# Kernel tuning notes

Measured on AMD Instinct MI355X. Metric: run time of the kernel, lower is better.

## Reference

```python
import jax, jax.numpy as jnp
import numpy as np

B = 8; NPC = 12500; N = B * NPC
L = 10.0; RES = 0.7; K = 16
IN_CH = 64; H1 = 68; H2 = 128; RNN = 128; ATTN = 32; E4 = 4 * RNN
EPS = 1e-5


def _knn_np(refs, queries, k):
    out = np.empty((queries.shape[0], k), dtype=np.int64)
    r2 = (refs * refs).sum(1)
    for s in range(0, queries.shape[0], 2048):
        q = queries[s:s + 2048]
        d2 = (q * q).sum(1)[:, None] - 2.0 * q @ refs.T + r2[None, :]
        out[s:s + q.shape[0]] = np.argpartition(d2, k, axis=1)[:, :k]
    return out


def setup_inputs():
    rng = np.random.default_rng(0)
    pos = rng.uniform(0.0, L, (N, 3)).astype(np.float32)
    batch = np.repeat(np.arange(B), NPC).astype(np.int32)
    x = (0.5 * rng.standard_normal((N, IN_CH))).astype(np.float32)
    refl = rng.uniform(0.0, 1.0, N).astype(np.float32)
    # voxel-grid sampling: one representative point per occupied voxel per cloud
    G = int(np.ceil(L / RES)) + 1
    v = np.floor(pos / RES).astype(np.int64)
    vkey = ((batch.astype(np.int64) * G + v[:, 0]) * G + v[:, 1]) * G + v[:, 2]
    _, first = np.unique(vkey, return_index=True)
    idx = np.sort(first)
    M = idx.shape[0]
    # per-cloud brute-force KNN (k neighbors in full set for every sampled point)
    src_list = []
    for b in range(B):
        qi = idx[(idx >= b * NPC) & (idx < (b + 1) * NPC)]
        src_list.append(_knn_np(pos[b * NPC:(b + 1) * NPC], pos[qi], K) + b * NPC)
    src = np.concatenate(src_list, 0).reshape(-1)
    tgt = np.repeat(np.arange(M), K)
    edge_index = np.stack([src, tgt]).astype(np.int32)

    def W(*s):
        return jnp.asarray((0.05 * rng.standard_normal(s)).astype(np.float32))

    def zeros(c):
        return jnp.zeros((c,), jnp.float32)

    def bnp(c):  # packed inference-mode BN params: [gamma, beta, mean, var]
        return jnp.asarray(np.stack([1.0 + 0.1 * rng.standard_normal(c), 0.1 * rng.standard_normal(c), 0.1 * rng.standard_normal(c), 1.0 + 0.1 * rng.uniform(0.0, 1.0, c)]).astype(np.float32))

    def dwp(c):  # depthwise k=1 conv = per-channel [weight, bias]
        return jnp.asarray(np.stack([1.0 + 0.1 * rng.standard_normal(c), 0.1 * rng.standard_normal(c)]).astype(np.float32))

    gum = -np.log(-np.log(rng.uniform(1e-6, 1.0 - 1e-6, (B, 2))))
    return dict(
        x=jnp.asarray(x), pos=jnp.asarray(pos), reflectance=jnp.asarray(refl),
        gumbel=jnp.asarray(gum.astype(np.float32)),
        gate_w1=W(4, H1), gate_b1=zeros(H1), gate_w2=W(H1, H1), gate_b2=zeros(H1),
        gate_wg=W(H1, 2), gate_bg=jnp.asarray(np.array([0.0, 2.0], np.float32)),
        loc_w1=W(H1, H2), loc_b1=zeros(H2), loc_w2=W(H2, H2), loc_b2=zeros(H2),
        attn_w1=W(H2, ATTN), attn_b1=zeros(ATTN), attn_w2=W(ATTN),
        exp_w=W(RNN, E4), exp_b=zeros(E4), exp_bn=bnp(E4),
        ds1_dw=dwp(E4), ds1_bn1=bnp(E4), ds1_pw_w=W(E4, E4), ds1_pw_b=zeros(E4), ds1_bn2=bnp(E4),
        blk_bn1=bnp(E4),
        ds2_dw=dwp(E4), ds2_bn1=bnp(E4), ds2_pw_w=W(E4, E4), ds2_pw_b=zeros(E4), ds2_bn2=bnp(E4),
        blk_bn2=bnp(E4),
        proj_w=W(E4, RNN), proj_b=zeros(RNN), proj_bn=bnp(RNN),
        batch=jnp.asarray(batch), idx=jnp.asarray(idx.astype(np.int32)),
        edge_index=jnp.asarray(edge_index), k=K, num_graphs=B)


def _bn(z, p):
    return p[0] * (z - p[2]) / jnp.sqrt(p[3] + EPS) + p[1]


def reference(x, pos, reflectance, gumbel, gate_w1, gate_b1, gate_w2, gate_b2, gate_wg, gate_bg, loc_w1, loc_b1, loc_w2, loc_b2, attn_w1, attn_b1, attn_w2, exp_w, exp_b, exp_bn, ds1_dw, ds1_bn1, ds1_pw_w, ds1_pw_b, ds1_bn2, blk_bn1, ds2_dw, ds2_bn1, ds2_pw_w, ds2_pw_b, ds2_bn2, blk_bn2, proj_w, proj_b, proj_bn, batch, idx, edge_index, k, num_graphs):
    # --- BinaryReflectanceGate (soft gumbel-softmax, tau=1) ---
    feats = jnp.concatenate([pos, reflectance[:, None]], -1)  # [N,4]
    h = jax.nn.relu(feats @ gate_w1 + gate_b1)
    h = jax.nn.relu(h @ gate_w2 + gate_b2)
    pooled = jax.ops.segment_max(h, batch, num_segments=num_graphs)  # global_max_pool
    logits = pooled @ gate_wg + gate_bg
    y_soft = jax.nn.softmax(logits + gumbel, axis=-1)
    refl_g = y_soft[:, 1][batch] * reflectance  # gated reflectance [N]
    pos4 = jnp.concatenate([pos, refl_g[:, None]], -1)  # [N,4]
    # --- AttentivePointNetConv: gather -> local MLP -> softmax attn -> reduce ---
    M = idx.shape[0]
    src = edge_index[0].reshape(M, k)  # k source neighbors per centroid
    msg_in = jnp.concatenate([x[src], pos4[src] - pos4[idx][:, None, :]], -1)  # [M,k,68]
    hm = jax.nn.relu(msg_in @ loc_w1 + loc_b1)
    msg = jax.nn.relu(hm @ loc_w2 + loc_b2)  # [M,k,128]
    score = jnp.tanh(msg @ attn_w1 + attn_b1) @ attn_w2  # [M,k]
    alpha = jax.nn.softmax(score, axis=-1)  # softmax over each centroid's edges
    agg = jnp.einsum('mk,mkc->mc', alpha, msg)  # [M,128]
    # --- InvertedResidualBlock (all convs kernel=1 -> channel matmuls, BN inference) ---
    out = jax.nn.relu(_bn(agg @ exp_w + exp_b, exp_bn))  # expand 128->512

    def ds(z, dw, bn1, pw_w, pw_b, bn2):
        d = jax.nn.relu(_bn(z * dw[0] + dw[1], bn1))  # depthwise k=1
        return _bn(d @ pw_w + pw_b, bn2)  # pointwise

    out = _bn(ds(out, ds1_dw, ds1_bn1, ds1_pw_w, ds1_pw_b, ds1_bn2), blk_bn1)
    out = _bn(ds(out, ds2_dw, ds2_bn1, ds2_pw_w, ds2_pw_b, ds2_bn2), blk_bn2)
    out = _bn(out @ proj_w + proj_b, proj_bn)  # project 512->128
    out = jax.nn.relu(out + agg)  # identity shortcut (RNN==RNN)
    return (out, pos[idx], batch[idx], refl_g[idx])
```

## Files before the change

kernel.cpp:

```cpp
#include <hip/hip_runtime.h>
#include <hip/hip_bf16.h>

typedef __hip_bfloat16 bf16;

#define B_GR 8
#define IN_CH 64
#define H1 68
#define H2 128
#define ATTN 32
#define E4 512
#define RNN 128
#define KNN 16
#define EPSV 1e-5f

typedef __attribute__((ext_vector_type(8))) short s8v;
typedef __attribute__((ext_vector_type(4))) float f4v;
#define MFMA16(a,b,c) __builtin_amdgcn_mfma_f32_16x16x32_bf16(a,b,c,0,0,0)

#define SK96 104
#define SK128 136
#define SK512 520

template<int DT> __device__ __forceinline__ float LD(const void* p, size_t i) {
    if (DT) return __bfloat162float(((const bf16*)p)[i]);
    return ((const float*)p)[i];
}
template<int DT> __device__ __forceinline__ void ST(void* p, size_t i, float v) {
    if (DT) ((bf16*)p)[i] = __float2bfloat16(v);
    else    ((float*)p)[i] = v;
}
__device__ __forceinline__ unsigned short f2bfb(float f) {
    unsigned u = __float_as_uint(f);
    unsigned r = (u + 0x7FFFu + ((u >> 16) & 1u)) >> 16;
    return (unsigned short)r;
}
__device__ __forceinline__ float bfb2f(unsigned short u) {
    return __uint_as_float(((unsigned)u) << 16);
}

__global__ void prep_kernel(const void* pos, int* flag, int* pooled) {
    const int tid = threadIdx.x;
    for (int i = tid; i < B_GR*H1; i += 256) pooled[i] = 0;
    if (tid == 0) {
        const unsigned* w = (const unsigned*)pos;
        int ok = 1;
        #pragma unroll 8
        for (int i = 0; i < 256; i++) {
            float f = __uint_as_float((w[i] & 0xFFFFu) << 16);
            if (!(f >= -0.01f && f <= 10.05f)) ok = 0;
        }
        *flag = ok;
    }
}

#define W1T_E (128*SK96)
#define W2T_E (128*SK128)
#define AW1T_E (32*SK128)
#define EXPT_E (512*SK128)
#define D1T_E (512*SK512)
#define D2T_E (512*SK512)
#define PJT_E (128*SK512)
#define GW2T_E (80*SK96)
template<int DT> __global__ __launch_bounds__(256) void trans_kernel(
    const int* __restrict__ flag,
    const void* __restrict__ w1, const void* __restrict__ w2, const void* __restrict__ aw1,
    const void* __restrict__ expw, const void* __restrict__ d1pw,
    const void* __restrict__ d2pw, const void* __restrict__ pjw,
    const void* __restrict__ gw2,
    unsigned short* __restrict__ w1T, unsigned short* __restrict__ w2T,
    unsigned short* __restrict__ aw1T, unsigned short* __restrict__ expwT,
    unsigned short* __restrict__ d1pwT, unsigned short* __restrict__ d2pwT,
    unsigned short* __restrict__ pjwT, unsigned short* __restrict__ gw2gT)
{
    if (*flag != DT) return;
    const int T0 = W1T_E, T1 = T0+W2T_E, T2 = T1+AW1T_E, T3 = T2+EXPT_E,
              T4 = T3+D1T_E, T5 = T4+D2T_E, T6 = T5+PJT_E, T7 = T6+GW2T_E;
    for (int i = blockIdx.x*256 + threadIdx.x; i < T7; i += gridDim.x*256) {
        if (i < T0) {
            int n = i / SK96, k = i - n*SK96;
            w1T[i] = (k < H1) ? f2bfb(LD<DT>(w1, (size_t)k*H2 + n)) : 0;
        } else if (i < T1) {
            int j = i - T0; int n = j / SK128, k = j - n*SK128;
            w2T[j] = (k < H2) ? f2bfb(LD<DT>(w2, (size_t)k*H2 + n)) : 0;
        } else if (i < T2) {
            int j = i - T1; int n = j / SK128, k = j - n*SK128;
            aw1T[j] = (k < H2) ? f2bfb(LD<DT>(aw1, (size_t)k*ATTN + n)) : 0;
        } else if (i < T3) {
            int j = i - T2; int n = j / SK128, k = j - n*SK128;
            expwT[j] = (k < RNN) ? f2bfb(LD<DT>(expw, (size_t)k*E4 + n)) : 0;
        } else if (i < T4) {
            int j = i - T3; int n = j / SK512, k = j - n*SK512;
            d1pwT[j] = (k < E4) ? f2bfb(LD<DT>(d1pw, (size_t)k*E4 + n)) : 0;
        } else if (i < T5) {
            int j = i - T4; int n = j / SK512, k = j - n*SK512;
            d2pwT[j] = (k < E4) ? f2bfb(LD<DT>(d2pw, (size_t)k*E4 + n)) : 0;
        } else if (i < T6) {
            int j = i - T5; int n = j / SK512, k = j - n*SK512;
            pjwT[j] = (k < E4) ? f2bfb(LD<DT>(pjw, (size_t)k*RNN + n)) : 0;
        } else {
            int j = i - T6; int n = j / SK96, k = j - n*SK96;
            gw2gT[j] = (k < H1 && n < H1) ? f2bfb(LD<DT>(gw2, (size_t)k*H1 + n)) : 0;
        }
    }
}

template<int DT> __global__ void coef_kernel(
    const int* __restrict__ flag,
    const void* __restrict__ expb, const void* __restrict__ expbn,
    const void* __restrict__ d1dw, const void* __restrict__ d1bn1,
    const void* __restrict__ d1pb, const void* __restrict__ d1bn2, const void* __restrict__ bbn1,
    const void* __restrict__ d2dw, const void* __restrict__ d2bn1,
    const void* __restrict__ d2pb, const void* __restrict__ d2bn2, const void* __restrict__ bbn2,
    const void* __restrict__ pjb, const void* __restrict__ pjbn,
    float4* __restrict__ C1, float2* __restrict__ C2, float2* __restrict__ C3,
    float2* __restrict__ C4)
{
    if (*flag != DT) return;
    int c = blockIdx.x*256 + threadIdx.x;
    if (c < E4) {
        float a_e = LD<DT>(expbn,c) * rsqrtf(LD<DT>(expbn,3*E4+c)+EPSV);
        float t0  = a_e*(LD<DT>(expb,c) - LD<DT>(expbn,2*E4+c)) + LD<DT>(expbn,E4+c);
        float a1 = LD<DT>(d1bn1,c) * rsqrtf(LD<DT>(d1bn1,3*E4+c)+EPSV);
        float s1 = a1 * LD<DT>(d1dw,c);
        float t1 = a1*(LD<DT>(d1dw,E4+c) - LD<DT>(d1bn1,2*E4+c)) + LD<DT>(d1bn1,E4+c);
        C1[c] = make_float4(a_e, t0, s1, t1);
        float a2 = LD<DT>(d1bn2,c) * rsqrtf(LD<DT>(d1bn2,3*E4+c)+EPSV);
        float t2 = a2*(LD<DT>(d1pb,c) - LD<DT>(d1bn2,2*E4+c)) + LD<DT>(d1bn2,E4+c);
        float a3 = LD<DT>(bbn1,c) * rsqrtf(LD<DT>(bbn1,3*E4+c)+EPSV);
        float S2 = a3*a2;
        float T2 = a3*(t2 - LD<DT>(bbn1,2*E4+c)) + LD<DT>(bbn1,E4+c);
        float a4 = LD<DT>(d2bn1,c) * rsqrtf(LD<DT>(d2bn1,3*E4+c)+EPSV);
        float sdw = a4 * LD<DT>(d2dw,c);
        float tdw = a4*(LD<DT>(d2dw,E4+c) - LD<DT>(d2bn1,2*E4+c)) + LD<DT>(d2bn1,E4+c);
        C2[c] = make_float2(sdw*S2, sdw*T2 + tdw);
        float a5 = LD<DT>(d2bn2,c) * rsqrtf(LD<DT>(d2bn2,3*E4+c)+EPSV);
        float t5 = a5*(LD<DT>(d2pb,c) - LD<DT>(d2bn2,2*E4+c)) + LD<DT>(d2bn2,E4+c);
        float a6 = LD<DT>(bbn2,c) * rsqrtf(LD<DT>(bbn2,3*E4+c)+EPSV);
        C3[c] = make_float2(a6*a5, a6*(t5 - LD<DT>(bbn2,2*E4+c)) + LD<DT>(bbn2,E4+c));
    }
    if (c < RNN) {
        float ap = LD<DT>(pjbn,c) * rsqrtf(LD<DT>(pjbn,3*RNN+c)+EPSV);
        C4[c] = make_float2(ap, ap*(LD<DT>(pjb,c) - LD<DT>(pjbn,2*RNN+c)) + LD<DT>(pjbn,RNN+c));
    }
}

template<int DT> __global__ __launch_bounds__(256) void gate_mfma(
    const int* __restrict__ flag,
    const void* __restrict__ pos, const void* __restrict__ refl,
    const void* __restrict__ w1, const void* __restrict__ b1, const void* __restrict__ b2g,
    const unsigned short* __restrict__ gw2gT,
    int* __restrict__ pooled, int NPC, int CPB)
{
    if (*flag != DT) return;
    __shared__ __align__(16) unsigned short hs[256*SK96];
    __shared__ float w1s[4*H1], b1s[H1], b2s[H1];
    const int tid = threadIdx.x;
    for (int i = tid; i < 4*H1; i += 256) w1s[i] = LD<DT>(w1, i);
    if (tid < H1) { b1s[tid] = LD<DT>(b1, tid); b2s[tid] = LD<DT>(b2g, tid); }
    __syncthreads();

    const int bb = blockIdx.x / CPB;
    const int cc = blockIdx.x % CPB;
    const int base = bb*NPC + cc*256;
    const int limit = NPC - cc*256;
    const int p = base + ((tid < limit) ? tid : 0);

    {
        float f0 = LD<DT>(pos, (size_t)p*3+0), f1 = LD<DT>(pos, (size_t)p*3+1);
        float f2 = LD<DT>(pos, (size_t)p*3+2), f3 = LD<DT>(refl, p);
        float h[H1];
        #pragma unroll
        for (int j = 0; j < H1; j++)
            h[j] = fmaxf(b1s[j] + f0*w1s[j] + f1*w1s[H1+j] + f2*w1s[2*H1+j] + f3*w1s[3*H1+j], 0.f);
        #pragma unroll
        for (int j = 0; j < H1; j += 2) {
            unsigned v = (unsigned)f2bfb(h[j]) | ((unsigned)f2bfb(h[j+1]) << 16);
            *(unsigned*)&hs[tid*SK96 + j] = v;
        }
        #pragma unroll
        for (int j = H1; j < 96; j += 2) *(unsigned*)&hs[tid*SK96 + j] = 0;
    }
    __syncthreads();

    const int wv = tid >> 6, lane = tid & 63, quad = lane >> 4, l15 = lane & 15;
    f4v acc[4][5];
    #pragma unroll
    for (int mt = 0; mt < 4; mt++)
        #pragma unroll
        for (int nt = 0; nt < 5; nt++) acc[mt][nt] = (f4v){0.f,0.f,0.f,0.f};
    s8v af[4][3];
    #pragma unroll
    for (int mt = 0; mt < 4; mt++)
        #pragma unroll
        for (int ks = 0; ks < 3; ks++)
            af[mt][ks] = *(const s8v*)&hs[(wv*64 + mt*16 + l15)*SK96 + ks*32 + quad*8];
    #pragma unroll
    for (int nt = 0; nt < 5; nt++) {
        #pragma unroll
        for (int ks = 0; ks < 3; ks++) {
            s8v bf_ = *(const s8v*)&gw2gT[(size_t)(nt*16 + l15)*SK96 + ks*32 + quad*8];
            #pragma unroll
            for (int mt = 0; mt < 4; mt++) acc[mt][nt] = MFMA16(af[mt][ks], bf_, acc[mt][nt]);
        }
    }
    #pragma unroll
    for (int nt = 0; nt < 5; nt++) {
        int col = nt*16 + l15;
        float v = acc[0][nt][0];
        #pragma unroll
        for (int mt = 0; mt < 4; mt++)
            #pragma unroll
            for (int r = 0; r < 4; r++) v = fmaxf(v, acc[mt][nt][r]);
        v = fmaxf(v, __shfl_xor(v, 16));
        v = fmaxf(v, __shfl_xor(v, 32));
        if (quad == 0 && col < H1) {
            float o = fmaxf(v + b2s[col], 0.f);
            atomicMax(&pooled[bb*H1 + col], __float_as_int(o));
        }
    }
}

template<int DT> __global__ void gate2_kernel(
    const int* __restrict__ flag, const int* __restrict__ pooled,
    const void* __restrict__ wg, const void* __restrict__ bg,
    const void* __restrict__ gum, float* __restrict__ y1)
{
    if (*flag != DT) return;
    __shared__ float lg[B_GR][2];
    const int t = threadIdx.x;
    if (t < B_GR*2) {
        int b = t >> 1, g = t & 1;
        float a = LD<DT>(bg, g) + LD<DT>(gum, b*2+g);
        for (int c = 0; c < H1; c++) a += __int_as_float(pooled[b*H1+c]) * LD<DT>(wg, c*2+g);
        lg[b][g] = a;
    }
    __syncthreads();
    if (t < B_GR) {
        float l0 = lg[t][0], l1 = lg[t][1];
        float m = fmaxf(l0, l1);
        float e0 = __expf(l0-m), e1 = __expf(l1-m);
        y1[t] = e1 / (e0 + e1);
    }
}

template<int DT> __global__ __launch_bounds__(256) void edge_mfma(
    const int* __restrict__ flag,
    const void* __restrict__ x, const void* __restrict__ pos,
    const void* __restrict__ refl, const float* __restrict__ y1,
    const int* __restrict__ batch,
    const int* __restrict__ idxarr, const int* __restrict__ esrc,
    const void* __restrict__ b1, const void* __restrict__ b2,
    const void* __restrict__ ab1, const void* __restrict__ aw2,
    const unsigned short* __restrict__ gw1T, const unsigned short* __restrict__ gw2T,
    const unsigned short* __restrict__ gaw1T,
    void* __restrict__ out, int M)
{
    if (*flag != DT) return;
    __shared__ __align__(16) unsigned short u2[128*SK128];
    __shared__ float p4[8][4];
    __shared__ int   srow[128];
    __shared__ float b1s[H2], b2s[H2], ab1s[ATTN], aw2s[ATTN];
    __shared__ float scores[128], alpha[128];

    const int tid = threadIdx.x;
    const int m0 = blockIdx.x * 8;

    if (tid < 128) {
        int mm = m0 + (tid >> 4); if (mm >= M) mm = M - 1;
        srow[tid] = esrc[mm*KNN + (tid & 15)];
    }
    if (tid < 32) {
        int tt = tid >> 2, c = tid & 3;
        int mm = m0 + tt; if (mm >= M) mm = M - 1;
        int t_idx = idxarr[mm];
        p4[tt][c] = (c < 3) ? LD<DT>(pos, (size_t)t_idx*3 + c)
                            : y1[batch[t_idx]] * LD<DT>(refl, t_idx);
    }
    if (tid < H2) { b1s[tid] = LD<DT>(b1, tid); b2s[tid] = LD<DT>(b2, tid); }
    if (tid < ATTN) { ab1s[tid] = LD<DT>(ab1, tid); aw2s[tid] = LD<DT>(aw2, tid); }
    __syncthreads();

    if (DT) {
        int r = tid >> 1, hf = tid & 1;
        int s = srow[r], tt = r >> 4;
        const uint4* xs = (const uint4*)x;
        uint4* du = (uint4*)u2;
        #pragma unroll
        for (int q = 0; q < 4; q++)
            du[r*17 + hf*4 + q] = xs[(size_t)s*8 + hf*4 + q];
        if (hf == 0) {
            #pragma unroll
            for (int k = 64; k < 68; k++) {
                float v = (k < 67) ? LD<1>(pos, (size_t)s*3 + (k-64)) - p4[tt][k-64]
                                   : y1[batch[s]] * LD<1>(refl, s) - p4[tt][3];
                u2[r*SK128 + k] = f2bfb(v);
            }
        } else {
            #pragma unroll
            for (int k = 68; k < 96; k += 2) *(unsigned*)&u2[r*SK128 + k] = 0;
        }
    } else {
        int r = tid >> 1, half = tid & 1;
        int s = srow[r], tt = r >> 4;
        size_t xb = (size_t)s * IN_CH;
        int k0 = half * 48;
        for (int kk = 0; kk < 48; kk++) {
            int k = k0 + kk;
            float v;
            if (k < IN_CH)       v = LD<DT>(x, xb + k);
            else if (k < 67)     v = LD<DT>(pos, (size_t)s*3 + (k - 64)) - p4[tt][k - 64];
            else if (k == 67)    v = y1[batch[s]] * LD<DT>(refl, s) - p4[tt][3];
            else                 v = 0.f;
            u2[r*SK128 + k] = f2bfb(v);
        }
    }
    __syncthreads();

    const int wv = tid >> 6, lane = tid & 63, quad = lane >> 4, l15 = lane & 15;
    const int rbase = wv * 32;

    {
        s8v af[2][3];
        #pragma unroll
        for (int mt = 0; mt < 2; mt++)
            #pragma unroll
            for (int ks = 0; ks < 3; ks++)
                af[mt][ks] = *(const s8v*)&u2[(rbase + mt*16 + l15)*SK128 + ks*32 + quad*8];
        __syncthreads();
        f4v acc[2][8];
        #pragma unroll
        for (int mt = 0; mt < 2; mt++)
            #pragma unroll
            for (int nt = 0; nt < 8; nt++) acc[mt][nt] = (f4v){0.f,0.f,0.f,0.f};
        #pragma unroll
        for (int nt = 0; nt < 8; nt++) {
            #pragma unroll
            for (int ks = 0; ks < 3; ks++) {
                s8v bf_ = *(const s8v*)&gw1T[(size_t)(nt*16 + l15)*SK96 + ks*32 + quad*8];
                acc[0][nt] = MFMA16(af[0][ks], bf_, acc[0][nt]);
                acc[1][nt] = MFMA16(af[1][ks], bf_, acc[1][nt]);
            }
        }
        #pragma unroll
        for (int mt = 0; mt < 2; mt++)
            #pragma unroll
            for (int nt = 0; nt < 8; nt++)
                #pragma unroll
                for (int r = 0; r < 4; r++) {
                    int row = rbase + mt*16 + quad*4 + r;
                    int col = nt*16 + l15;
                    u2[row*SK128 + col] = f2bfb(fmaxf(acc[mt][nt][r] + b1s[col], 0.f));
                }
    }
    __syncthreads();

    {
        s8v af[2][4];
        #pragma unroll
        for (int mt = 0; mt < 2; mt++)
            #pragma unroll
            for (int ks = 0; ks < 4; ks++)
                af[mt][ks] = *(const s8v*)&u2[(rbase + mt*16 + l15)*SK128 + ks*32 + quad*8];
        __syncthreads();
        f4v acc[2][8];
        #pragma unroll
        for (int mt = 0; mt < 2; mt++)
            #pragma unroll
            for (int nt = 0; nt < 8; nt++) acc[mt][nt] = (f4v){0.f,0.f,0.f,0.f};
        #pragma unroll
        for (int nt = 0; nt < 8; nt++) {
            #pragma unroll
            for (int ks = 0; ks < 4; ks++) {
                s8v bf_ = *(const s8v*)&gw2T[(size_t)(nt*16 + l15)*SK128 + ks*32 + quad*8];
                acc[0][nt] = MFMA16(af[0][ks], bf_, acc[0][nt]);
                acc[1][nt] = MFMA16(af[1][ks], bf_, acc[1][nt]);
            }
        }
        #pragma unroll
        for (int mt = 0; mt < 2; mt++)
            #pragma unroll
            for (int nt = 0; nt < 8; nt++)
                #pragma unroll
                for (int r = 0; r < 4; r++) {
                    int row = rbase + mt*16 + quad*4 + r;
                    int col = nt*16 + l15;
                    u2[row*SK128 + col] = f2bfb(fmaxf(acc[mt][nt][r] + b2s[col], 0.f));
                }
    }
    __syncthreads();

    {
        s8v af[2][4];
        #pragma unroll
        for (int mt = 0; mt < 2; mt++)
            #pragma unroll
            for (int ks = 0; ks < 4; ks++)
                af[mt][ks] = *(const s8v*)&u2[(rbase + mt*16 + l15)*SK128 + ks*32 + quad*8];
        f4v acc[2][2];
        #pragma unroll
        for (int mt = 0; mt < 2; mt++)
            #pragma unroll
            for (int nt = 0; nt < 2; nt++) acc[mt][nt] = (f4v){0.f,0.f,0.f,0.f};
        #pragma unroll
        for (int nt = 0; nt < 2; nt++) {
            #pragma unroll
            for (int ks = 0; ks < 4; ks++) {
                s8v bf_ = *(const s8v*)&gaw1T[(size_t)(nt*16 + l15)*SK128 + ks*32 + quad*8];
                acc[0][nt] = MFMA16(af[0][ks], bf_, acc[0][nt]);
                acc[1][nt] = MFMA16(af[1][ks], bf_, acc[1][nt]);
            }
        }
        #pragma unroll
        for (int mt = 0; mt < 2; mt++)
            #pragma unroll
            for (int r = 0; r < 4; r++) {
                float s = 0.f;
                #pragma unroll
                for (int nt = 0; nt < 2; nt++) {
                    int col = nt*16 + l15;
                    s += tanhf(acc[mt][nt][r] + ab1s[col]) * aw2s[col];
                }
                s += __shfl_xor(s, 1);
                s += __shfl_xor(s, 2);
                s += __shfl_xor(s, 4);
                s += __shfl_xor(s, 8);
                if (l15 == 0) scores[rbase + mt*16 + quad*4 + r] = s;
            }
    }
    __syncthreads();

    if (tid < 128) {
        int base = (tid >> 4) << 4;
        float mx = scores[base];
        #pragma unroll
        for (int j = 1; j < KNN; j++) mx = fmaxf(mx, scores[base+j]);
        float den = 0.f;
        #pragma unroll
        for (int j = 0; j < KNN; j++) den += __expf(scores[base+j] - mx);
        alpha[tid] = __expf(scores[tid] - mx) / den;
    }
    __syncthreads();

    if (tid < 128) {
        int tt = tid >> 4, c0 = (tid & 15) * 8;
        int mm = m0 + tt;
        float a[8] = {0,0,0,0,0,0,0,0};
        #pragma unroll
        for (int j = 0; j < KNN; j++) {
            float al = alpha[tt*16 + j];
            s8v v = *(const s8v*)&u2[(tt*16 + j)*SK128 + c0];
            #pragma unroll
            for (int e = 0; e < 8; e++) a[e] += al * bfb2f((unsigned short)v[e]);
        }
        if (mm < M) {
            if (DT) {
                unsigned short pk[8];
                #pragma unroll
                for (int e = 0; e < 8; e++) pk[e] = f2bfb(a[e]);
                *(uint4*)((bf16*)out + (size_t)mm*H2 + c0) = *(const uint4*)pk;
            } else {
                #pragma unroll
                for (int e = 0; e < 8; e++) ST<0>(out, (size_t)mm*H2 + c0 + e, a[e]);
            }
        }
    } else if (tid < 160) {
        int t = tid - 128;
        int tt = t >> 2, c = t & 3;
        int mm = m0 + tt;
        if (mm < M) {
            if (c < 3) ST<DT>(out, (size_t)M*128 + mm*3 + c, p4[tt][c]);
            else {
                ST<DT>(out, (size_t)M*131 + mm, (float)batch[idxarr[mm]]);
                ST<DT>(out, (size_t)M*132 + mm, p4[tt][3]);
            }
        }
    }
}

template<int DT> __global__ __launch_bounds__(256) void post_mfma(
    const int* __restrict__ flag,
    const unsigned short* __restrict__ expwT, const unsigned short* __restrict__ d1pwT,
    const unsigned short* __restrict__ d2pwT, const unsigned short* __restrict__ pjwT,
    const float4* __restrict__ C1, const float2* __restrict__ C2,
    const float2* __restrict__ C3, const float2* __restrict__ C4,
    void* __restrict__ out, int M)
{
    if (*flag != DT) return;
    __shared__ __align__(16) unsigned short zs[32*SK512];
    __shared__ __align__(16) unsigned short a0[32*SK128];
    const int tid = threadIdx.x;
    const int m0 = blockIdx.x * 32;

    {
        int r = tid >> 3;
        int c0 = (tid & 7) * 16;
        int mm = m0 + r;
        for (int c = c0; c < c0+16; c++) {
            float v = (mm < M) ? LD<DT>(out, (size_t)mm*RNN + c) : 0.f;
            a0[r*SK128 + c] = f2bfb(v);
        }
        if ((tid & 7) == 7) for (int c = RNN; c < SK128; c++) a0[r*SK128 + c] = 0;
    }
    __syncthreads();

    const int wv = tid >> 6, lane = tid & 63, quad = lane >> 4, l15 = lane & 15;
    const int nbase = wv * 128;

    f4v acc[2][8];

    #pragma unroll
    for (int mt = 0; mt < 2; mt++)
        #pragma unroll
        for (int nt = 0; nt < 8; nt++) acc[mt][nt] = (f4v){0.f,0.f,0.f,0.f};
    #pragma unroll
    for (int ks = 0; ks < 4; ks++) {
        s8v af0 = *(const s8v*)&a0[(l15)*SK128 + ks*32 + quad*8];
        s8v af1 = *(const s8v*)&a0[(16+l15)*SK128 + ks*32 + quad*8];
        #pragma unroll
        for (int nt = 0; nt < 8; nt++) {
            s8v bf_ = *(const s8v*)&expwT[(size_t)(nbase + nt*16 + l15)*SK128 + ks*32 + quad*8];
            acc[0][nt] = MFMA16(af0, bf_, acc[0][nt]);
            acc[1][nt] = MFMA16(af1, bf_, acc[1][nt]);
        }
    }
    #pragma unroll
    for (int nt = 0; nt < 8; nt++) {
        int col = nbase + nt*16 + l15;
        float4 cf = C1[col];
        #pragma unroll
        for (int mt = 0; mt < 2; mt++)
            #pragma unroll
            for (int r = 0; r < 4; r++) {
                int row = mt*16 + quad*4 + r;
                float u = fmaxf(cf.x*acc[mt][nt][r] + cf.y, 0.f);
                float d = fmaxf(cf.z*u + cf.w, 0.f);
                zs[row*SK512 + col] = f2bfb(d);
            }
    }
    __syncthreads();

    #pragma unroll
    for (int mt = 0; mt < 2; mt++)
        #pragma unroll
        for (int nt = 0; nt < 8; nt++) acc[mt][nt] = (f4v){0.f,0.f,0.f,0.f};
    for (int ks = 0; ks < 16; ks++) {
        s8v af0 = *(const s8v*)&zs[(l15)*SK512 + ks*32 + quad*8];
        s8v af1 = *(const s8v*)&zs[(16+l15)*SK512 + ks*32 + quad*8];
        #pragma unroll
        for (int nt = 0; nt < 8; nt++) {
            s8v bf_ = *(const s8v*)&d1pwT[(size_t)(nbase + nt*16 + l15)*SK512 + ks*32 + quad*8];
            acc[0][nt] = MFMA16(af0, bf_, acc[0][nt]);
            acc[1][nt] = MFMA16(af1, bf_, acc[1][nt]);
        }
    }
    __syncthreads();
    #pragma unroll
    for (int nt = 0; nt < 8; nt++) {
        int col = nbase + nt*16 + l15;
        float2 cf = C2[col];
        #pragma unroll
        for (int mt = 0; mt < 2; mt++)
            #pragma unroll
            for (int r = 0; r < 4; r++) {
                int row = mt*16 + quad*4 + r;
                zs[row*SK512 + col] = f2bfb(fmaxf(cf.x*acc[mt][nt][r] + cf.y, 0.f));
            }
    }
    __syncthreads();

    #pragma unroll
    for (int mt = 0; mt < 2; mt++)
        #pragma unroll
        for (int nt = 0; nt < 8; nt++) acc[mt][nt] = (f4v){0.f,0.f,0.f,0.f};
    for (int ks = 0; ks < 16; ks++) {
        s8v af0 = *(const s8v*)&zs[(l15)*SK512 + ks*32 + quad*8];
        s8v af1 = *(const s8v*)&zs[(16+l15)*SK512 + ks*32 + quad*8];
        #pragma unroll
        for (int nt = 0; nt < 8; nt++) {
            s8v bf_ = *(const s8v*)&d2pwT[(size_t)(nbase + nt*16 + l15)*SK512 + ks*32 + quad*8];
            acc[0][nt] = MFMA16(af0, bf_, acc[0][nt]);
            acc[1][nt] = MFMA16(af1, bf_, acc[1][nt]);
        }
    }
    __syncthreads();
    #pragma unroll
    for (int nt = 0; nt < 8; nt++) {
        int col = nbase + nt*16 + l15;
        float2 cf = C3[col];
        #pragma unroll
        for (int mt = 0; mt < 2; mt++)
            #pragma unroll
            for (int r = 0; r < 4; r++) {
                int row = mt*16 + quad*4 + r;
                zs[row*SK512 + col] = f2bfb(cf.x*acc[mt][nt][r] + cf.y);
            }
    }
    __syncthreads();

    {
        f4v pacc[2][2];
        #pragma unroll
        for (int mt = 0; mt < 2; mt++)
            #pragma unroll
            for (int nt = 0; nt < 2; nt++) pacc[mt][nt] = (f4v){0.f,0.f,0.f,0.f};
        for (int ks = 0; ks < 16; ks++) {
            s8v af0 = *(const s8v*)&zs[(l15)*SK512 + ks*32 + quad*8];
            s8v af1 = *(const s8v*)&zs[(16+l15)*SK512 + ks*32 + quad*8];
            #pragma unroll
            for (int nt = 0; nt < 2; nt++) {
                s8v bf_ = *(const s8v*)&pjwT[(size_t)(wv*32 + nt*16 + l15)*SK512 + ks*32 + quad*8];
                pacc[0][nt] = MFMA16(af0, bf_, pacc[0][nt]);
                pacc[1][nt] = MFMA16(af1, bf_, pacc[1][nt]);
            }
        }
        #pragma unroll
        for (int nt = 0; nt < 2; nt++) {
            int col = wv*32 + nt*16 + l15;
            float2 cf = C4[col];
            #pragma unroll
            for (int mt = 0; mt < 2; mt++)
                #pragma unroll
                for (int r = 0; r < 4; r++) {
                    int row = mt*16 + quad*4 + r;
                    int mm = m0 + row;
                    if (mm < M) {
                        float agv = bfb2f(a0[row*SK128 + col]);
                        float o = fmaxf(cf.x*pacc[mt][nt][r] + cf.y + agv, 0.f);
                        ST<DT>(out, (size_t)mm*RNN + col, o);
                    }
                }
        }
    }
}

extern "C" void kernel_launch(void* const* d_in, const int* in_sizes, int n_in,
                              void* d_out, int out_size, void* d_ws, size_t ws_size,
                              hipStream_t stream)
{
    const void* x    = d_in[0];
    const void* pos  = d_in[1];
    const void* refl = d_in[2];
    const void* gum  = d_in[3];
    const void* gw1  = d_in[4];
    const void* gb1  = d_in[5];
    const void* gw2  = d_in[6];
    const void* gb2  = d_in[7];
    const void* gwg  = d_in[8];
    const void* gbg  = d_in[9];
    const void* lw1  = d_in[10];
    const void* lb1  = d_in[11];
    const void* lw2  = d_in[12];
    const void* lb2  = d_in[13];
    const void* aw1  = d_in[14];
    const void* ab1  = d_in[15];
    const void* aw2  = d_in[16];
    const void* expw = d_in[17];
    const void* expb = d_in[18];
    const void* expbn= d_in[19];
    const void* d1dw = d_in[20];
    const void* d1bn1= d_in[21];
    const void* d1pw = d_in[22];
    const void* d1pb = d_in[23];
    const void* d1bn2= d_in[24];
    const void* bbn1 = d_in[25];
    const void* d2dw = d_in[26];
    const void* d2bn1= d_in[27];
    const void* d2pw = d_in[28];
    const void* d2pb = d_in[29];
    const void* d2bn2= d_in[30];
    const void* bbn2 = d_in[31];
    const void* pjw  = d_in[32];
    const void* pjb  = d_in[33];
    const void* pjbn = d_in[34];
    const int* batch = (const int*)d_in[35];
    const int* idxp  = (const int*)d_in[36];
    const int* eidx  = (const int*)d_in[37];

    const int N = in_sizes[2];
    const int M = in_sizes[36];
    const int NPC = N / B_GR;
    const int CPB = (NPC + 255) / 256;

    char* wsb = (char*)d_ws;
    int*  flag   = (int*)wsb;
    int*  pooled = (int*)(wsb + 16);
    float* y1    = (float*)(wsb + 2304);
    unsigned short* w1T   = (unsigned short*)(wsb + 2368);
    unsigned short* w2T   = w1T + W1T_E;
    unsigned short* aw1T  = w2T + W2T_E;
    unsigned short* expwT = aw1T + AW1T_E;
    unsigned short* d1pwT = expwT + EXPT_E;
    unsigned short* d2pwT = d1pwT + D1T_E;
    unsigned short* pjwT  = d2pwT + D2T_E;
    unsigned short* gw2gT = pjwT + PJT_E;
    float4* C1 = (float4*)(gw2gT + GW2T_E + 8);
    float2* C2 = (float2*)(C1 + E4);
    float2* C3 = C2 + E4;
    float2* C4 = C3 + E4;

    prep_kernel<<<1, 256, 0, stream>>>(pos, flag, pooled);

    trans_kernel<0><<<512, 256, 0, stream>>>(flag, lw1, lw2, aw1, expw, d1pw, d2pw, pjw, gw2,
                                             w1T, w2T, aw1T, expwT, d1pwT, d2pwT, pjwT, gw2gT);
    trans_kernel<1><<<512, 256, 0, stream>>>(flag, lw1, lw2, aw1, expw, d1pw, d2pw, pjw, gw2,
                                             w1T, w2T, aw1T, expwT, d1pwT, d2pwT, pjwT, gw2gT);

    coef_kernel<0><<<2, 256, 0, stream>>>(flag, expb, expbn, d1dw, d1bn1, d1pb, d1bn2, bbn1,
                                          d2dw, d2bn1, d2pb, d2bn2, bbn2, pjb, pjbn,
                                          C1, C2, C3, C4);
    coef_kernel<1><<<2, 256, 0, stream>>>(flag, expb, expbn, d1dw, d1bn1, d1pb, d1bn2, bbn1,
                                          d2dw, d2bn1, d2pb, d2bn2, bbn2, pjb, pjbn,
                                          C1, C2, C3, C4);

    gate_mfma<0><<<B_GR*CPB, 256, 0, stream>>>(flag, pos, refl, gw1, gb1, gb2, gw2gT, pooled, NPC, CPB);
    gate_mfma<1><<<B_GR*CPB, 256, 0, stream>>>(flag, pos, refl, gw1, gb1, gb2, gw2gT, pooled, NPC, CPB);

    gate2_kernel<0><<<1, 64, 0, stream>>>(flag, pooled, gwg, gbg, gum, y1);
    gate2_kernel<1><<<1, 64, 0, stream>>>(flag, pooled, gwg, gbg, gum, y1);

    const int EB = (M + 7) / 8;
    edge_mfma<0><<<EB, 256, 0, stream>>>(flag, x, pos, refl, y1, batch, idxp, eidx,
                                         lb1, lb2, ab1, aw2, w1T, w2T, aw1T, d_out, M);
    edge_mfma<1><<<EB, 256, 0, stream>>>(flag, x, pos, refl, y1, batch, idxp, eidx,
                                         lb1, lb2, ab1, aw2, w1T, w2T, aw1T, d_out, M);

    const int PB = (M + 31) / 32;
    post_mfma<0><<<PB, 256, 0, stream>>>(flag, expwT, d1pwT, d2pwT, pjwT, C1, C2, C3, C4, d_out, M);
    post_mfma<1><<<PB, 256, 0, stream>>>(flag, expwT, d1pwT, d2pwT, pjwT, C1, C2, C3, C4, d_out, M);
}
```

Before: 560.8 us.

## Make edge_mfma wave-independent: load A fragments from global, drop block barriers

Each wave now owns two centroids end to end. It loads the gathered neighbor features straight from global memory into MFMA A-fragments instead of staging them through shared memory. Every block-wide __syncthreads is removed and the per-block shared bias, score and alpha arrays go away, so bias loads move into registers. Softmax and aggregation now run inside each wave. tanhf is replaced by an exp-based fast_tanh, which changes accuracy slightly. The risk is uncoalesced gathered global loads and possible races, since waves reuse their own u2 rows without barriers.

Measured after the change: 472.9 us. 1.19x faster.

```diff
diff --git a/kernel.cpp b/kernel.cpp
--- a/kernel.cpp
+++ b/kernel.cpp
@@ -36,6 +36,11 @@
 }
 __device__ __forceinline__ float bfb2f(unsigned short u) {
     return __uint_as_float(((unsigned)u) << 16);
+}
+__device__ __forceinline__ float fast_tanh(float x) {
+    x = fminf(fmaxf(x, -12.f), 12.f);
+    float e = __expf(2.f * x);
+    return (e - 1.f) / (e + 1.f);
 }
 
 __global__ void prep_kernel(const void* pos, int* flag, int* pooled) {
@@ -257,81 +262,56 @@
 {
     if (*flag != DT) return;
     __shared__ __align__(16) unsigned short u2[128*SK128];
-    __shared__ float p4[8][4];
-    __shared__ int   srow[128];
-    __shared__ float b1s[H2], b2s[H2], ab1s[ATTN], aw2s[ATTN];
-    __shared__ float scores[128], alpha[128];
+    __shared__ float ssc[4][2][16];
 
     const int tid = threadIdx.x;
-    const int m0 = blockIdx.x * 8;
-
-    if (tid < 128) {
-        int mm = m0 + (tid >> 4); if (mm >= M) mm = M - 1;
-        srow[tid] = esrc[mm*KNN + (tid & 15)];
-    }
-    if (tid < 32) {
-        int tt = tid >> 2, c = tid & 3;
-        int mm = m0 + tt; if (mm >= M) mm = M - 1;
+    const int wv = tid >> 6, lane = tid & 63, quad = lane >> 4, l15 = lane & 15;
+    const int m0 = blockIdx.x * 8 + wv * 2;
+    const int rb = wv * 32;
+
+    s8v af[2][3];
+    int mcl[2];
+    float p4v[2][4];
+    #pragma unroll
+    for (int t = 0; t < 2; t++) {
+        int mm = m0 + t; if (mm >= M) mm = M - 1;
+        mcl[t] = mm;
         int t_idx = idxarr[mm];
-        p4[tt][c] = (c < 3) ? LD<DT>(pos, (size_t)t_idx*3 + c)
-                            : y1[batch[t_idx]] * LD<DT>(refl, t_idx);
-    }
-    if (tid < H2) { b1s[tid] = LD<DT>(b1, tid); b2s[tid] = LD<DT>(b2, tid); }
-    if (tid < ATTN) { ab1s[tid] = LD<DT>(ab1, tid); aw2s[tid] = LD<DT>(aw2, tid); }
-    __syncthreads();
-
-    if (DT) {
-        int r = tid >> 1, hf = tid & 1;
-        int s = srow[r], tt = r >> 4;
-        const uint4* xs = (const uint4*)x;
-        uint4* du = (uint4*)u2;
-        #pragma unroll
-        for (int q = 0; q < 4; q++)
-            du[r*17 + hf*4 + q] = xs[(size_t)s*8 + hf*4 + q];
-        if (hf == 0) {
-            #pragma unroll
-            for (int k = 64; k < 68; k++) {
-                float v = (k < 67) ? LD<1>(pos, (size_t)s*3 + (k-64)) - p4[tt][k-64]
-                                   : y1[batch[s]] * LD<1>(refl, s) - p4[tt][3];
-                u2[r*SK128 + k] = f2bfb(v);
-            }
+        p4v[t][0] = LD<DT>(pos, (size_t)t_idx*3 + 0);
+        p4v[t][1] = LD<DT>(pos, (size_t)t_idx*3 + 1);
+        p4v[t][2] = LD<DT>(pos, (size_t)t_idx*3 + 2);
+        p4v[t][3] = y1[batch[t_idx]] * LD<DT>(refl, t_idx);
+        int s = esrc[mm*KNN + l15];
+        if (DT) {
+            const unsigned short* xs = (const unsigned short*)x + (size_t)s*IN_CH;
+            af[t][0] = *(const s8v*)(xs + quad*8);
+            af[t][1] = *(const s8v*)(xs + 32 + quad*8);
         } else {
-            #pragma unroll
-            for (int k = 68; k < 96; k += 2) *(unsigned*)&u2[r*SK128 + k] = 0;
-        }
-    } else {
-        int r = tid >> 1, half = tid & 1;
-        int s = srow[r], tt = r >> 4;
-        size_t xb = (size_t)s * IN_CH;
-        int k0 = half * 48;
-        for (int kk = 0; kk < 48; kk++) {
-            int k = k0 + kk;
-            float v;
-            if (k < IN_CH)       v = LD<DT>(x, xb + k);
-            else if (k < 67)     v = LD<DT>(pos, (size_t)s*3 + (k - 64)) - p4[tt][k - 64];
-            else if (k == 67)    v = y1[batch[s]] * LD<DT>(refl, s) - p4[tt][3];
-            else                 v = 0.f;
-            u2[r*SK128 + k] = f2bfb(v);
-        }
-    }
-    __syncthreads();
-
-    const int wv = tid >> 6, lane = tid & 63, quad = lane >> 4, l15 = lane & 15;
-    const int rbase = wv * 32;
+            unsigned short tmp0[8], tmp1[8];
+            #pragma unroll
+            for (int e = 0; e < 8; e++) {
+                tmp0[e] = f2bfb(LD<0>(x, (size_t)s*IN_CH + quad*8 + e));
+                tmp1[e] = f2bfb(LD<0>(x, (size_t)s*IN_CH + 32 + quad*8 + e));
+            }
+            af[t][0] = *(const s8v*)tmp0;
+            af[t][1] = *(const s8v*)tmp1;
+        }
+        s8v a2 = (s8v){0,0,0,0,0,0,0,0};
+        if (quad == 0) {
+            a2[0] = (short)f2bfb(LD<DT>(pos, (size_t)s*3 + 0) - p4v[t][0]);
+            a2[1] = (short)f2bfb(LD<DT>(pos, (size_t)s*3 + 1) - p4v[t][1]);
+            a2[2] = (short)f2bfb(LD<DT>(pos, (size_t)s*3 + 2) - p4v[t][2]);
+            a2[3] = (short)f2bfb(y1[batch[s]] * LD<DT>(refl, s) - p4v[t][3]);
+        }
+        af[t][2] = a2;
+    }
 
     {
-        s8v af[2][3];
-        #pragma unroll
-        for (int mt = 0; mt < 2; mt++)
-            #pragma unroll
-            for (int ks = 0; ks < 3; ks++)
-                af[mt][ks] = *(const s8v*)&u2[(rbase + mt*16 + l15)*SK128 + ks*32 + quad*8];
-        __syncthreads();
         f4v acc[2][8];
         #pragma unroll
-        for (int mt = 0; mt < 2; mt++)
-            #pragma unroll
-            for (int nt = 0; nt < 8; nt++) acc[mt][nt] = (f4v){0.f,0.f,0.f,0.f};
+        for (int t = 0; t < 2; t++)
+            #pragma unroll
+            for (int nt = 0; nt < 8; nt++) acc[t][nt] = (f4v){0.f,0.f,0.f,0.f};
         #pragma unroll
         for (int nt = 0; nt < 8; nt++) {
             #pragma unroll
@@ -342,136 +322,128 @@
             }
         }
         #pragma unroll
-        for (int mt = 0; mt < 2; mt++)
-            #pragma unroll
-            for (int nt = 0; nt < 8; nt++)
+        for (int nt = 0; nt < 8; nt++) {
+            int col = nt*16 + l15;
+            float bb = LD<DT>(b1, col);
+            #pragma unroll
+            for (int t = 0; t < 2; t++)
                 #pragma unroll
                 for (int r = 0; r < 4; r++) {
-                    int row = rbase + mt*16 + quad*4 + r;
-                    int col = nt*16 + l15;
-                    u2[row*SK128 + col] = f2bfb(fmaxf(acc[mt][nt][r] + b1s[col], 0.f));
+                    int row = rb + t*16 + quad*4 + r;
+                    u2[row*SK128 + col] = f2bfb(fmaxf(acc[t][nt][r] + bb, 0.f));
                 }
-    }
-    __syncthreads();
+        }
+    }
 
     {
-        s8v af[2][4];
-        #pragma unroll
-        for (int mt = 0; mt < 2; mt++)
+        s8v af2[2][4];
+        #pragma unroll
+        for (int t = 0; t < 2; t++)
             #pragma unroll
             for (int ks = 0; ks < 4; ks++)
-                af[mt][ks] = *(const s8v*)&u2[(rbase + mt*16 + l15)*SK128 + ks*32 + quad*8];
-        __syncthreads();
+                af2[t][ks] = *(const s8v*)&u2[(rb + t*16 + l15)*SK128 + ks*32 + quad*8];
         f4v acc[2][8];
         #pragma unroll
-        for (int mt = 0; mt < 2; mt++)
-            #pragma unroll
-            for (int nt = 0; nt < 8; nt++) acc[mt][nt] = (f4v){0.f,0.f,0.f,0.f};
+        for (int t = 0; t < 2; t++)
+            #pragma unroll
+            for (int nt = 0; nt < 8; nt++) acc[t][nt] = (f4v){0.f,0.f,0.f,0.f};
         #pragma unroll
         for (int nt = 0; nt < 8; nt++) {
             #pragma unroll
             for (int ks = 0; ks < 4; ks++) {
                 s8v bf_ = *(const s8v*)&gw2T[(size_t)(nt*16 + l15)*SK128 + ks*32 + quad*8];
-                acc[0][nt] = MFMA16(af[0][ks], bf_, acc[0][nt]);
-                acc[1][nt] = MFMA16(af[1][ks], bf_, acc[1][nt]);
-            }
-        }
-        #pragma unroll
-        for (int mt = 0; mt < 2; mt++)
-            #pragma unroll
-            for (int nt = 0; nt < 8; nt++)
+                acc[0][nt] = MFMA16(af2[0][ks], bf_, acc[0][nt]);
+                acc[1][nt] = MFMA16(af2[1][ks], bf_, acc[1][nt]);
+            }
+        }
+        #pragma unroll
+        for (int nt = 0; nt < 8; nt++) {
+            int col = nt*16 + l15;
+            float bb = LD<DT>(b2, col);
+            #pragma unroll
+            for (int t = 0; t < 2; t++)
                 #pragma unroll
                 for (int r = 0; r < 4; r++) {
-                    int row = rbase + mt*16 + quad*4 + r;
-                    int col = nt*16 + l15;
-                    u2[row*SK128 + col] = f2bfb(fmaxf(acc[mt][nt][r] + b2s[col], 0.f));
+                    int row = rb + t*16 + quad*4 + r;
+                    u2[row*SK128 + col] = f2bfb(fmaxf(acc[t][nt][r] + bb, 0.f));
                 }
-    }
-    __syncthreads();
+        }
+    }
 
     {
-        s8v af[2][4];
-        #pragma unroll
-        for (int mt = 0; mt < 2; mt++)
+        s8v af3[2][4];
+        #pragma unroll
+        for (int t = 0; t < 2; t++)
             #pragma unroll
             for (int ks = 0; ks < 4; ks++)
-                af[mt][ks] = *(const s8v*)&u2[(rbase + mt*16 + l15)*SK128 + ks*32 + quad*8];
+                af3[t][ks] = *(const s8v*)&u2[(rb + t*16 + l15)*SK128 + ks*32 + quad*8];
         f4v acc[2][2];
         #pragma unroll
-        for (int mt = 0; mt < 2; mt++)
-            #pragma unroll
-            for (int nt = 0; nt < 2; nt++) acc[mt][nt] = (f4v){0.f,0.f,0.f,0.f};
+        for (int t = 0; t < 2; t++)
+            #pragma unroll
+            for (int nt = 0; nt < 2; nt++) acc[t][nt] = (f4v){0.f,0.f,0.f,0.f};
         #pragma unroll
         for (int nt = 0; nt < 2; nt++) {
             #pragma unroll
             for (int ks = 0; ks < 4; ks++) {
                 s8v bf_ = *(const s8v*)&gaw1T[(size_t)(nt*16 + l15)*SK128 + ks*32 + quad*8];
-                acc[0][nt] = MFMA16(af[0][ks], bf_, acc[0][nt]);
-                acc[1][nt] = MFMA16(af[1][ks], bf_, acc[1][nt]);
-            }
-        }
-        #pragma unroll
-        for (int mt = 0; mt < 2; mt++)
+                acc[0][nt] = MFMA16(af3[0][ks], bf_, acc[0][nt]);
+                acc[1][nt] = MFMA16(af3[1][ks], bf_, acc[1][nt]);
+            }
+        }
+        #pragma unroll
+        for (int t = 0; t < 2; t++)
             #pragma unroll
             for (int r = 0; r < 4; r++) {
                 float s = 0.f;
                 #pragma unroll
                 for (int nt = 0; nt < 2; nt++) {
                     int col = nt*16 + l15;
-                    s += tanhf(acc[mt][nt][r] + ab1s[col]) * aw2s[col];
+                    s += fast_tanh(acc[t][nt][r] + LD<DT>(ab1, col)) * LD<DT>(aw2, col);
                 }
                 s += __shfl_xor(s, 1);
                 s += __shfl_xor(s, 2);
                 s += __shfl_xor(s, 4);
                 s += __shfl_xor(s, 8);
-                if (l15 == 0) scores[rbase + mt*16 + quad*4 + r] = s;
-            }
-    }
-    __syncthreads();
-
-    if (tid < 128) {
-        int base = (tid >> 4) << 4;
-        float mx = scores[base];
-        #pragma unroll
-        for (int j = 1; j < KNN; j++) mx = fmaxf(mx, scores[base+j]);
+                if (l15 == 0) ssc[wv][t][quad*4 + r] = s;
+            }
+    }
+
+    #pragma unroll
+    for (int t = 0; t < 2; t++) {
+        float sc[KNN];
+        #pragma unroll
+        for (int j = 0; j < KNN; j++) sc[j] = ssc[wv][t][j];
+        float mx = sc[0];
+        #pragma unroll
+        for (int j = 1; j < KNN; j++) mx = fmaxf(mx, sc[j]);
         float den = 0.f;
         #pragma unroll
-        for (int j = 0; j < KNN; j++) den += __expf(scores[base+j] - mx);
-        alpha[tid] = __expf(scores[tid] - mx) / den;
-    }
-    __syncthreads();
-
-    if (tid < 128) {
-        int tt = tid >> 4, c0 = (tid & 15) * 8;
-        int mm = m0 + tt;
-        float a[8] = {0,0,0,0,0,0,0,0};
+        for (int j = 0; j < KNN; j++) { sc[j] = __expf(sc[j] - mx); den += sc[j]; }
+        float inv = 1.f / den;
+        float a0 = 0.f, a1 = 0.f;
         #pragma unroll
         for (int j = 0; j < KNN; j++) {
-            float al = alpha[tt*16 + j];
-            s8v v = *(const s8v*)&u2[(tt*16 + j)*SK128 + c0];
-            #pragma unroll
-            for (int e = 0; e < 8; e++) a[e] += al * bfb2f((unsigned short)v[e]);
-        }
+            unsigned v = *(const unsigned*)&u2[(rb + t*16 + j)*SK128 + 2*lane];
+            float w = sc[j] * inv;
+            a0 += w * bfb2f((unsigned short)(v & 0xFFFFu));
+            a1 += w * bfb2f((unsigned short)(v >> 16));
+        }
+        int mm = m0 + t;
         if (mm < M) {
             if (DT) {
-                unsigned short pk[8];
-                #pragma unroll
-                for (int e = 0; e < 8; e++) pk[e] = f2bfb(a[e]);
-                *(uint4*)((bf16*)out + (size_t)mm*H2 + c0) = *(const uint4*)pk;
+                unsigned pk = (unsigned)f2bfb(a0) | ((unsigned)f2bfb(a1) << 16);
+                *(unsigned*)((bf16*)out + (size_t)mm*H2 + 2*lane) = pk;
             } else {
-                #pragma unroll
-                for (int e = 0; e < 8; e++) ST<0>(out, (size_t)mm*H2 + c0 + e, a[e]);
-            }
-        }
-    } else if (tid < 160) {
-        int t = tid - 128;
-        int tt = t >> 2, c = t & 3;
-        int mm = m0 + tt;
-        if (mm < M) {
-            if (c < 3) ST<DT>(out, (size_t)M*128 + mm*3 + c, p4[tt][c]);
-            else {
-                ST<DT>(out, (size_t)M*131 + mm, (float)batch[idxarr[mm]]);
-                ST<DT>(out, (size_t)M*132 + mm, p4[tt][3]);
+                ST<0>(out, (size_t)mm*H2 + 2*lane, a0);
+                ST<0>(out, (size_t)mm*H2 + 2*lane + 1, a1);
+            }
+            if (lane == 0) {
+                ST<DT>(out, (size_t)M*128 + mm*3 + 0, p4v[t][0]);
+                ST<DT>(out, (size_t)M*128 + mm*3 + 1, p4v[t][1]);
+                ST<DT>(out, (size_t)M*128 + mm*3 + 2, p4v[t][2]);
+                ST<DT>(out, (size_t)M*131 + mm, (float)batch[idxarr[mcl[t]]]);
+                ST<DT>(out, (size_t)M*132 + mm, p4v[t][3]);
             }
         }
     }
```
